# Kernel tuning notes

Hardware: AMD Instinct MI355X
Metric: run time of the kernel (lower is better)

## Reference

```python
import jax, jax.numpy as jnp
import numpy as np

WS = 7          # window size (square)
HEADS = 8
HEAD_DIM = 32
SCALE = HEAD_DIM ** -0.5

def _relative_indices():
    # static [49,49,2] indices into the (2*WS-1)^2 bias table, values in [0, 2*WS-2]
    idx = np.array([[x, y] for x in range(WS) for y in range(WS)])  # [49,2]
    rel = idx[None, :, :] - idx[:, None, :]                          # [49,49,2], in [-6,6]
    rel = rel - rel.min()                                            # shift to [0,12]
    return rel

_REL = _relative_indices()

def setup_inputs() -> dict:
    key = jax.random.key(0)
    ks = jax.random.split(key, 5)
    dim, inner = 256, HEADS * HEAD_DIM
    return {
        "x": jax.random.normal(ks[0], (32, 56, 56, dim), dtype=jnp.float32),
        "w_qkv": jax.random.normal(ks[1], (dim, 3 * inner), dtype=jnp.float32) * (dim ** -0.5),
        "w_out": jax.random.normal(ks[2], (inner, dim), dtype=jnp.float32) * (inner ** -0.5),
        "b_out": jax.random.normal(ks[3], (dim,), dtype=jnp.float32) * 0.01,
        "pos_emb": jax.random.normal(ks[4], (2 * WS - 1, 2 * WS - 1), dtype=jnp.float32),
    }

def _to_windows(t):
    # [b, nwh*WS, nww*WS, heads*d] -> [b, heads, nwh*nww, WS*WS, d]
    b, H, W, _ = t.shape
    nwh, nww = H // WS, W // WS
    t = t.reshape(b, nwh, WS, nww, WS, HEADS, HEAD_DIM)
    t = t.transpose(0, 5, 1, 3, 2, 4, 6)  # b h nwh nww wh ww d
    return t.reshape(b, HEADS, nwh * nww, WS * WS, HEAD_DIM)

def reference(x, w_qkv, w_out, b_out, pos_emb):
    b, H, W, _ = x.shape
    nwh, nww = H // WS, W // WS
    qkv = x @ w_qkv                                  # [b,H,W,3*inner]
    q, k, v = jnp.split(qkv, 3, axis=-1)
    q, k, v = _to_windows(q), _to_windows(k), _to_windows(v)  # [b,h,w,49,d]
    dots = jnp.einsum('bhwid,bhwjd->bhwij', q, k) * SCALE      # [b,h,w,49,49]
    bias = pos_emb[_REL[:, :, 0], _REL[:, :, 1]]               # gathered [49,49]
    attn = jax.nn.softmax(dots + bias, axis=-1)
    out = jnp.einsum('bhwij,bhwjd->bhwid', attn, v)            # [b,h,w,49,d]
    out = out.reshape(b, HEADS, nwh, nww, WS, WS, HEAD_DIM)
    out = out.transpose(0, 2, 4, 3, 5, 1, 6)                   # b nwh wh nww ww h d
    out = out.reshape(b, H, W, HEADS * HEAD_DIM)
    return out @ w_out + b_out
```

## Files before the change

kernel.cpp:

```cpp
#include <hip/hip_runtime.h>
#include <hip/hip_bf16.h>
#include <stdint.h>

typedef __attribute__((ext_vector_type(8))) short bf16x8;
typedef __attribute__((ext_vector_type(4))) float f32x4;
typedef __attribute__((ext_vector_type(16))) float f32x16;

#define AS1(p) ((const __attribute__((address_space(1))) void*)(p))
#define AS3(p) ((__attribute__((address_space(3))) void*)(p))

static __device__ __forceinline__ unsigned short f2bf(float f) {
  union { float f; unsigned u; } v; v.f = f;
  unsigned r = v.u + 0x7fffu + ((v.u >> 16) & 1u);
  return (unsigned short)(r >> 16);
}
static __device__ __forceinline__ float f4get(float4 v, int r) {
  return r == 0 ? v.x : r == 1 ? v.y : r == 2 ? v.z : v.w;
}
static __device__ __forceinline__ int grow(int rowbase, int t) {
  return rowbase + (t / 7) * 56 + (t % 7);
}

__global__ __launch_bounds__(256) void cast_x_kernel(const float* __restrict__ x,
                                                     unsigned short* __restrict__ xb,
                                                     int n4) {
  int idx = blockIdx.x * 256 + threadIdx.x;
  int stride = gridDim.x * 256;
  for (int i = idx; i < n4; i += stride) {
    float4 v = ((const float4*)x)[i];
    ushort4 o;
    o.x = f2bf(v.x); o.y = f2bf(v.y); o.z = f2bf(v.z); o.w = f2bf(v.w);
    ((ushort4*)xb)[i] = o;
  }
}

__global__ __launch_bounds__(256) void prep_w_kernel(const float* __restrict__ wqkv,
                                                     const float* __restrict__ wout,
                                                     unsigned short* __restrict__ wqkvT,
                                                     unsigned short* __restrict__ woutT) {
  int id = blockIdx.x * 256 + threadIdx.x;
  if (id < 768 * 256) {
    int n = id >> 8, k = id & 255;
    float v = wqkv[k * 768 + n];
    if (n < 256) v *= 0.17677669529663687f;
    wqkvT[id] = f2bf(v);
  } else {
    int id2 = id - 768 * 256;
    int n = id2 >> 8, k = id2 & 255;
    woutT[id2] = f2bf(wout[k * 256 + n]);
  }
}

template <int N_COLS, bool OUT_F32, bool BIAS>
__global__ __launch_bounds__(256) void gemm_kernel(const unsigned short* __restrict__ A,
                                                   const unsigned short* __restrict__ Bt,
                                                   void* __restrict__ Cout,
                                                   const float* __restrict__ bias) {
  constexpr int K = 256;
  constexpr int NB = N_COLS / 128;
  __shared__ __align__(16) unsigned short lA[128 * 64];
  __shared__ __align__(16) unsigned short lB[128 * 64];
  const int tid = threadIdx.x;
  const int lane = tid & 63;
  const int wid = tid >> 6;
  const int wr = wid >> 1, wc = wid & 1;

  const int orig = blockIdx.x;
  const int cpx = gridDim.x >> 3;
  const int swz = (orig & 7) * cpx + (orig >> 3);
  const int m0 = (swz / NB) * 128;
  const int n0 = (swz % NB) * 128;

  f32x4 acc[4][4];
#pragma unroll
  for (int i = 0; i < 4; ++i)
#pragma unroll
    for (int j = 0; j < 4; ++j) acc[i][j] = (f32x4){0.f, 0.f, 0.f, 0.f};

  for (int k0 = 0; k0 < K; k0 += 64) {
#pragma unroll
    for (int i = 0; i < 4; ++i) {
      int cidx = i * 256 + tid;
      int r = cidx >> 3, cc = cidx & 7;
      int scc = cc ^ (r & 7);
      const unsigned short* g = A + (size_t)(m0 + r) * K + k0 + scc * 8;
      __builtin_amdgcn_global_load_lds(AS1(g), AS3(&lA[cidx * 8]), 16, 0, 0);
    }
#pragma unroll
    for (int i = 0; i < 4; ++i) {
      int cidx = i * 256 + tid;
      int r = cidx >> 3, cc = cidx & 7;
      int scc = cc ^ (r & 7);
      const unsigned short* g = Bt + (size_t)(n0 + r) * K + k0 + scc * 8;
      __builtin_amdgcn_global_load_lds(AS1(g), AS3(&lB[cidx * 8]), 16, 0, 0);
    }
    __syncthreads();
#pragma unroll
    for (int kk = 0; kk < 2; ++kk) {
      bf16x8 af[4], bfr[4];
#pragma unroll
      for (int mi = 0; mi < 4; ++mi) {
        int r = wr * 64 + mi * 16 + (lane & 15);
        int kc = kk * 4 + (lane >> 4);
        int pc = kc ^ (r & 7);
        af[mi] = *reinterpret_cast<const bf16x8*>(&lA[r * 64 + pc * 8]);
      }
#pragma unroll
      for (int ni = 0; ni < 4; ++ni) {
        int r = wc * 64 + ni * 16 + (lane & 15);
        int kc = kk * 4 + (lane >> 4);
        int pc = kc ^ (r & 7);
        bfr[ni] = *reinterpret_cast<const bf16x8*>(&lB[r * 64 + pc * 8]);
      }
#pragma unroll
      for (int mi = 0; mi < 4; ++mi)
#pragma unroll
        for (int ni = 0; ni < 4; ++ni)
          acc[mi][ni] = __builtin_amdgcn_mfma_f32_16x16x32_bf16(af[mi], bfr[ni],
                                                                acc[mi][ni], 0, 0, 0);
    }
    __syncthreads();
  }

  const int rif = (lane >> 4) * 4;
  const int cif = lane & 15;
#pragma unroll
  for (int mi = 0; mi < 4; ++mi) {
#pragma unroll
    for (int ni = 0; ni < 4; ++ni) {
      int col = n0 + wc * 64 + ni * 16 + cif;
      float bv = BIAS ? bias[col] : 0.f;
#pragma unroll
      for (int j = 0; j < 4; ++j) {
        int row = m0 + wr * 64 + mi * 16 + rif + j;
        float v = acc[mi][ni][j] + bv;
        if (OUT_F32)
          ((float*)Cout)[(size_t)row * N_COLS + col] = v;
        else
          ((unsigned short*)Cout)[(size_t)row * N_COLS + col] = f2bf(v);
      }
    }
  }
}

__global__ __launch_bounds__(256) void attn_mfma_kernel(const unsigned short* __restrict__ qkv,
                                                        const float* __restrict__ pe,
                                                        unsigned short* __restrict__ aout) {
  __shared__ float biasL[64 * 64];
  __shared__ unsigned short Vt[4][32 * 72];
  const int tid = threadIdx.x;

  for (int id = tid; id < 4096; id += 256) {
    int i = id >> 6, j = id & 63;
    float v = 0.f;
    if (i < 49 && j < 49) {
      int xi = i / 7, yi = i % 7, xj = j / 7, yj = j % 7;
      v = pe[(xj - xi + 6) * 13 + (yj - yi + 6)];
    }
    biasL[i * 64 + ((((unsigned)j >> 2) ^ (i & 15)) << 2) + (j & 3)] = v;
  }
  __syncthreads();

  const int lane = tid & 63;
  const int wv = tid >> 6;
  const int hi = lane >> 5;
  const int l31 = lane & 31;
  const int h = blockIdx.y * 4 + wv;
  const int win = blockIdx.x;
  const int rowbase = (win >> 6) * 3136 + ((win & 63) >> 3) * 392 + (win & 7) * 7;
  unsigned short* vt = Vt[wv];

  const int vrow = lane < 49 ? lane : 48;
  const unsigned short* vpr = qkv + (size_t)grow(rowbase, vrow) * 768 + h * 32 + 512;
  bf16x8 vr[4];
#pragma unroll
  for (int t = 0; t < 4; ++t) vr[t] = *(const bf16x8*)(vpr + t * 8);
  if (lane >= 49) {
#pragma unroll
    for (int t = 0; t < 4; ++t) vr[t] = bf16x8{0, 0, 0, 0, 0, 0, 0, 0};
  }

  bf16x8 qf[2][2], kf[2][2];
#pragma unroll
  for (int t = 0; t < 2; ++t) {
    int r = t * 32 + l31; if (r > 48) r = 48;
    const unsigned short* base = qkv + (size_t)grow(rowbase, r) * 768 + h * 32;
#pragma unroll
    for (int ks = 0; ks < 2; ++ks) {
      qf[t][ks] = *(const bf16x8*)(base + ks * 16 + hi * 8);
      kf[t][ks] = *(const bf16x8*)(base + 256 + ks * 16 + hi * 8);
    }
  }

  f32x16 acc[2][2];
#pragma unroll
  for (int mi = 0; mi < 2; ++mi)
#pragma unroll
    for (int ni = 0; ni < 2; ++ni) {
#pragma unroll
      for (int z = 0; z < 16; ++z) acc[mi][ni][z] = 0.f;
#pragma unroll
      for (int ks = 0; ks < 2; ++ks)
        acc[mi][ni] = __builtin_amdgcn_mfma_f32_32x32x16_bf16(kf[mi][ks], qf[ni][ks],
                                                              acc[mi][ni], 0, 0, 0);
    }

#pragma unroll
  for (int t = 0; t < 4; ++t)
#pragma unroll
    for (int e = 0; e < 8; ++e)
      vt[(t * 8 + e) * 72 + lane] = (unsigned short)vr[t][e];

  unsigned int pkw[2][2][4][2];
#pragma unroll
  for (int ni = 0; ni < 2; ++ni) {
    const int i = ni * 32 + l31;
    float s[32];
    float m = -3e38f;
#pragma unroll
    for (int mi = 0; mi < 2; ++mi)
#pragma unroll
      for (int q = 0; q < 4; ++q) {
        int cc = (mi * 8 + q * 2 + hi) ^ (i & 15);
        float4 b4 = *(const float4*)&biasL[i * 64 + cc * 4];
#pragma unroll
        for (int r = 0; r < 4; ++r) {
          float v = acc[mi][ni][q * 4 + r] + f4get(b4, r);
          s[mi * 16 + q * 4 + r] = v;
          int j0 = mi * 32 + q * 8 + r;
          if (j0 + 4 * hi < 49) m = fmaxf(m, v);
        }
      }
    m = fmaxf(m, __shfl_xor(m, 32, 64));
    float sum = 0.f;
#pragma unroll
    for (int mi = 0; mi < 2; ++mi)
#pragma unroll
      for (int q = 0; q < 4; ++q)
#pragma unroll
        for (int r = 0; r < 4; ++r) {
          int j0 = mi * 32 + q * 8 + r;
          int idx = mi * 16 + q * 4 + r;
          float e = (j0 + 4 * hi < 49) ? __expf(s[idx] - m) : 0.f;
          s[idx] = e;
          sum += e;
        }
    sum += __shfl_xor(sum, 32, 64);
    float inv = 1.f / sum;
#pragma unroll
    for (int mi = 0; mi < 2; ++mi)
#pragma unroll
      for (int q = 0; q < 4; ++q)
#pragma unroll
        for (int w = 0; w < 2; ++w) {
          float lo = s[mi * 16 + q * 4 + 2 * w] * inv;
          float hp = s[mi * 16 + q * 4 + 2 * w + 1] * inv;
          unsigned int d;
          asm("v_cvt_pk_bf16_f32 %0, %1, %2" : "=v"(d) : "v"(lo), "v"(hp));
          pkw[ni][mi][q][w] = d;
        }
  }

  bf16x8 vfr[4];
#pragma unroll
  for (int ks = 0; ks < 4; ++ks)
    vfr[ks] = *(const bf16x8*)&vt[l31 * 72 + ks * 16 + hi * 8];

  f32x16 oacc[2];
#pragma unroll
  for (int oi = 0; oi < 2; ++oi) {
#pragma unroll
    for (int z = 0; z < 16; ++z) oacc[oi][z] = 0.f;
#pragma unroll
    for (int ks = 0; ks < 4; ++ks) {
      unsigned int a0 = pkw[oi][ks >> 1][(ks & 1) * 2][0];
      unsigned int a1 = pkw[oi][ks >> 1][(ks & 1) * 2][1];
      unsigned int b0 = pkw[oi][ks >> 1][(ks & 1) * 2 + 1][0];
      unsigned int b1 = pkw[oi][ks >> 1][(ks & 1) * 2 + 1][1];
      asm("v_permlane32_swap_b32 %0, %1" : "+v"(a0), "+v"(b0));
      asm("v_permlane32_swap_b32 %0, %1" : "+v"(a1), "+v"(b1));
      union { unsigned int u[4]; bf16x8 v; } pf;
      pf.u[0] = a0; pf.u[1] = a1; pf.u[2] = b0; pf.u[3] = b1;
      oacc[oi] = __builtin_amdgcn_mfma_f32_32x32x16_bf16(pf.v, vfr[ks], oacc[oi], 0, 0, 0);
    }
  }

#pragma unroll
  for (int oi = 0; oi < 2; ++oi)
#pragma unroll
    for (int reg = 0; reg < 16; ++reg) {
      int i = oi * 32 + (reg & 3) + 8 * (reg >> 2) + 4 * hi;
      if (i < 49)
        aout[(size_t)grow(rowbase, i) * 256 + h * 32 + l31] = f2bf(oacc[oi][reg]);
    }
}

extern "C" void kernel_launch(void* const* d_in, const int* in_sizes, int n_in,
                              void* d_out, int out_size, void* d_ws, size_t ws_size,
                              hipStream_t stream) {
  const float* x       = (const float*)d_in[0];
  const float* w_qkv   = (const float*)d_in[1];
  const float* w_out   = (const float*)d_in[2];
  const float* b_out   = (const float*)d_in[3];
  const float* pos_emb = (const float*)d_in[4];
  float* out = (float*)d_out;

  const int M = 32 * 56 * 56;
  char* ws = (char*)d_ws;
  unsigned short* xb    = (unsigned short*)ws;
  unsigned short* qkv   = (unsigned short*)(ws + 51380224);
  unsigned short* aout  = (unsigned short*)(ws + 51380224 + 154140672);
  unsigned short* wqkvT = (unsigned short*)(ws + 256901120);
  unsigned short* woutT = (unsigned short*)(ws + 257294336);

  cast_x_kernel<<<dim3(2048), dim3(256), 0, stream>>>(x, xb, M * 256 / 4);
  prep_w_kernel<<<dim3(1024), dim3(256), 0, stream>>>(w_qkv, w_out, wqkvT, woutT);
  gemm_kernel<768, false, false><<<dim3((M / 128) * 6), dim3(256), 0, stream>>>(xb, wqkvT, qkv, nullptr);
  attn_mfma_kernel<<<dim3(2048, 2), dim3(256), 0, stream>>>(qkv, pos_emb, aout);
  gemm_kernel<256, true, true><<<dim3((M / 128) * 2), dim3(256), 0, stream>>>(aout, woutT, out, b_out);
}
```

Baseline: 326.2 us.

## Fuse fp32-to-bf16 cast of x into QKV GEMM and widen attention blocks

Removes the separate cast kernel: the QKV GEMM now loads fp32 x directly, converts it to bf16 in registers and writes it into swizzled LDS. This saves a full write and read of the bf16 copy of x. Each N-tile re-reads and re-converts the fp32 A tile though, doubling A read bytes per tile and losing the async global-to-LDS path. The attention kernel also switches to 512-thread blocks that cover all 8 heads per window, so the bias table is built once per window instead of twice.

```diff
diff --git a/kernel.cpp b/kernel.cpp
--- a/kernel.cpp
+++ b/kernel.cpp
@@ -19,19 +19,6 @@
 }
 static __device__ __forceinline__ int grow(int rowbase, int t) {
   return rowbase + (t / 7) * 56 + (t % 7);
-}
-
-__global__ __launch_bounds__(256) void cast_x_kernel(const float* __restrict__ x,
-                                                     unsigned short* __restrict__ xb,
-                                                     int n4) {
-  int idx = blockIdx.x * 256 + threadIdx.x;
-  int stride = gridDim.x * 256;
-  for (int i = idx; i < n4; i += stride) {
-    float4 v = ((const float4*)x)[i];
-    ushort4 o;
-    o.x = f2bf(v.x); o.y = f2bf(v.y); o.z = f2bf(v.z); o.w = f2bf(v.w);
-    ((ushort4*)xb)[i] = o;
-  }
 }
 
 __global__ __launch_bounds__(256) void prep_w_kernel(const float* __restrict__ wqkv,
@@ -51,8 +38,8 @@
   }
 }
 
-template <int N_COLS, bool OUT_F32, bool BIAS>
-__global__ __launch_bounds__(256) void gemm_kernel(const unsigned short* __restrict__ A,
+template <int N_COLS, bool CAST_A, bool OUT_F32, bool BIAS>
+__global__ __launch_bounds__(256) void gemm_kernel(const void* __restrict__ Ain,
                                                    const unsigned short* __restrict__ Bt,
                                                    void* __restrict__ Cout,
                                                    const float* __restrict__ bias) {
@@ -78,13 +65,38 @@
     for (int j = 0; j < 4; ++j) acc[i][j] = (f32x4){0.f, 0.f, 0.f, 0.f};
 
   for (int k0 = 0; k0 < K; k0 += 64) {
-#pragma unroll
-    for (int i = 0; i < 4; ++i) {
-      int cidx = i * 256 + tid;
-      int r = cidx >> 3, cc = cidx & 7;
-      int scc = cc ^ (r & 7);
-      const unsigned short* g = A + (size_t)(m0 + r) * K + k0 + scc * 8;
-      __builtin_amdgcn_global_load_lds(AS1(g), AS3(&lA[cidx * 8]), 16, 0, 0);
+    if (CAST_A) {
+      const float* Af = (const float*)Ain;
+      float4 u[4][2];
+#pragma unroll
+      for (int i = 0; i < 4; ++i) {
+        int cidx = i * 256 + tid;
+        int r = cidx >> 3, cc = cidx & 7;
+        int scc = cc ^ (r & 7);
+        const float* g = Af + (size_t)(m0 + r) * K + k0 + scc * 8;
+        u[i][0] = ((const float4*)g)[0];
+        u[i][1] = ((const float4*)g)[1];
+      }
+#pragma unroll
+      for (int i = 0; i < 4; ++i) {
+        int cidx = i * 256 + tid;
+        union { unsigned short s[8]; bf16x8 v; } pk;
+        pk.s[0] = f2bf(u[i][0].x); pk.s[1] = f2bf(u[i][0].y);
+        pk.s[2] = f2bf(u[i][0].z); pk.s[3] = f2bf(u[i][0].w);
+        pk.s[4] = f2bf(u[i][1].x); pk.s[5] = f2bf(u[i][1].y);
+        pk.s[6] = f2bf(u[i][1].z); pk.s[7] = f2bf(u[i][1].w);
+        *reinterpret_cast<bf16x8*>(&lA[cidx * 8]) = pk.v;
+      }
+    } else {
+      const unsigned short* Ab = (const unsigned short*)Ain;
+#pragma unroll
+      for (int i = 0; i < 4; ++i) {
+        int cidx = i * 256 + tid;
+        int r = cidx >> 3, cc = cidx & 7;
+        int scc = cc ^ (r & 7);
+        const unsigned short* g = Ab + (size_t)(m0 + r) * K + k0 + scc * 8;
+        __builtin_amdgcn_global_load_lds(AS1(g), AS3(&lA[cidx * 8]), 16, 0, 0);
+      }
     }
 #pragma unroll
     for (int i = 0; i < 4; ++i) {
@@ -143,14 +155,14 @@
   }
 }
 
-__global__ __launch_bounds__(256) void attn_mfma_kernel(const unsigned short* __restrict__ qkv,
+__global__ __launch_bounds__(512) void attn_mfma_kernel(const unsigned short* __restrict__ qkv,
                                                         const float* __restrict__ pe,
                                                         unsigned short* __restrict__ aout) {
   __shared__ float biasL[64 * 64];
-  __shared__ unsigned short Vt[4][32 * 72];
+  __shared__ unsigned short Vt[8][32 * 72];
   const int tid = threadIdx.x;
 
-  for (int id = tid; id < 4096; id += 256) {
+  for (int id = tid; id < 4096; id += 512) {
     int i = id >> 6, j = id & 63;
     float v = 0.f;
     if (i < 49 && j < 49) {
@@ -165,7 +177,7 @@
   const int wv = tid >> 6;
   const int hi = lane >> 5;
   const int l31 = lane & 31;
-  const int h = blockIdx.y * 4 + wv;
+  const int h = wv;
   const int win = blockIdx.x;
   const int rowbase = (win >> 6) * 3136 + ((win & 63) >> 3) * 392 + (win & 7) * 7;
   unsigned short* vt = Vt[wv];
@@ -307,15 +319,13 @@
 
   const int M = 32 * 56 * 56;
   char* ws = (char*)d_ws;
-  unsigned short* xb    = (unsigned short*)ws;
-  unsigned short* qkv   = (unsigned short*)(ws + 51380224);
-  unsigned short* aout  = (unsigned short*)(ws + 51380224 + 154140672);
-  unsigned short* wqkvT = (unsigned short*)(ws + 256901120);
-  unsigned short* woutT = (unsigned short*)(ws + 257294336);
-
-  cast_x_kernel<<<dim3(2048), dim3(256), 0, stream>>>(x, xb, M * 256 / 4);
+  unsigned short* qkv   = (unsigned short*)ws;
+  unsigned short* aout  = (unsigned short*)(ws + 154140672);
+  unsigned short* wqkvT = (unsigned short*)(ws + 205520896);
+  unsigned short* woutT = (unsigned short*)(ws + 205914112);
+
   prep_w_kernel<<<dim3(1024), dim3(256), 0, stream>>>(w_qkv, w_out, wqkvT, woutT);
-  gemm_kernel<768, false, false><<<dim3((M / 128) * 6), dim3(256), 0, stream>>>(xb, wqkvT, qkv, nullptr);
-  attn_mfma_kernel<<<dim3(2048, 2), dim3(256), 0, stream>>>(qkv, pos_emb, aout);
-  gemm_kernel<256, true, true><<<dim3((M / 128) * 2), dim3(256), 0, stream>>>(aout, woutT, out, b_out);
-}
+  gemm_kernel<768, true, false, false><<<dim3((M / 128) * 6), dim3(256), 0, stream>>>(x, wqkvT, qkv, nullptr);
+  attn_mfma_kernel<<<dim3(2048), dim3(512), 0, stream>>>(qkv, pos_emb, aout);
+  gemm_kernel<256, false, true, true><<<dim3((M / 128) * 2), dim3(256), 0, stream>>>(aout, woutT, out, b_out);
+}
```

New measurement: 347.5 us. 6.5% more time.
